# Kernel optimization log

Measured on AMD Instinct MI355X. Metric: run time of the kernel, lower is better.

Reference implementation:

```python
import jax, jax.numpy as jnp
import numpy as np
from jax import lax

BZ = 1024; ROI = 116; DIM = 116; FLAT = ROI * DIM
TOPK = 8; TEMP = 0.07; ALPHA = 0.1; A_COEF = 0.9; BETA = 2; EPS = 1e-5


def _leaky(v):
    return jnp.where(v >= 0, v, 0.2 * v)


def _bn2d(h, g, b):
    # training-mode BatchNorm1d on [N, C] (biased variance)
    m = h.mean(0)
    v = h.var(0)
    return (h - m) * lax.rsqrt(v + EPS) * g + b


def setup_inputs():
    key = jax.random.key(0)
    ks = jax.random.split(key, 16)
    def w(k, shape, s=0.05):
        return jax.random.normal(k, shape, jnp.float32) * s
    return {
        "x": jax.random.normal(ks[0], (BZ, ROI, DIM), jnp.float32),
        "pseudo": jax.random.normal(ks[1], (BZ, ROI, DIM), jnp.float32),
        "ages": jax.random.randint(ks[2], (BZ,), 0, 80, jnp.int32),
        "genders": jax.random.randint(ks[3], (BZ,), 0, 2, jnp.int32),
        "site": jax.random.randint(ks[4], (BZ, 4), 0, 10, jnp.int32),
        "fc_p_w": w(ks[5], (ROI, ROI)), "fc_p_b": jnp.zeros((ROI,), jnp.float32),
        "proj_w1": w(ks[6], (FLAT, ROI), 0.01), "proj_b1": jnp.zeros((ROI,), jnp.float32),
        "proj_w2": w(ks[7], (ROI, ROI)), "proj_b2": jnp.zeros((ROI,), jnp.float32),
        "gcn_w1": w(ks[8], (DIM, ROI)), "gcn_b1": jnp.zeros((ROI,), jnp.float32),
        "gcn_w2": w(ks[9], (ROI, ROI)), "gcn_b2": jnp.zeros((ROI,), jnp.float32),
        "gcn1_w": w(ks[10], (ROI, ROI)), "gcn1_b": jnp.zeros((ROI,), jnp.float32),
        "gcn2_w1": w(ks[11], (ROI, 64)), "gcn2_b1": jnp.zeros((64,), jnp.float32),
        "gcn2_w2": w(ks[12], (64, 8)), "gcn2_b2": jnp.zeros((8,), jnp.float32),
        "bn1_g": jnp.ones((ROI,), jnp.float32), "bn1_b": jnp.zeros((ROI,), jnp.float32),
        "bn2_g": jnp.ones((ROI,), jnp.float32), "bn2_b": jnp.zeros((ROI,), jnp.float32),
        "bn3_g": jnp.ones((ROI,), jnp.float32), "bn3_b": jnp.zeros((ROI,), jnp.float32),
    }


def _forward(x, pseudo, fc_p_w, fc_p_b, proj_w1, proj_b1, proj_w2, proj_b2,
             gcn_w1, gcn_b1, gcn_w2, gcn_b2, gcn1_w, gcn1_b,
             gcn2_w1, gcn2_b1, gcn2_w2, gcn2_b2,
             bn1_g, bn1_b, bn2_g, bn2_b, bn3_g, bn3_b,
             pos_idx, neg_idx, cond):
    bz = x.shape[0]
    pseudo = _leaky(pseudo @ fc_p_w + fc_p_b)
    x = x + pseudo                               # [bz, roi, dim]
    xf = x.reshape(bz, -1)                       # [bz, roi*dim]
    # contrastive head: Linear-ReLU-Linear, L2-normalize, cosine sim / temp
    p = jnp.maximum(xf @ proj_w1 + proj_b1, 0.0) @ proj_w2 + proj_b2
    pn = p / jnp.linalg.norm(p, axis=1, keepdims=True)
    sim = (pn @ pn.T) / TEMP                     # [bz, bz]
    sflat = sim.ravel()
    # -log(exp(pos)/(exp(pos)+exp(neg))) == softplus(neg - pos), truncated pairing
    loss = jnp.mean(jax.nn.softplus(sflat[neg_idx] - sflat[pos_idx]))
    sim_n = (sim - sim.min()) / (sim.max() - sim.min())
    # adjacency build: original does it in detached numpy -> stop_gradient
    xd = lax.stop_gradient(xf)
    sd = lax.stop_gradient(sim_n)
    sq = jnp.sum(xd * xd, axis=1)
    d2 = jnp.maximum(sq[:, None] + sq[None, :] - 2.0 * (xd @ xd.T), 0.0)
    fsim = jnp.exp(-ALPHA * jnp.sqrt(d2))
    total = fsim * (1.0 - sd) + sd
    dist = total * jnp.where(cond, A_COEF, 1.0 - A_COEF)
    vals, idxs = lax.top_k(dist, TOPK)           # row-wise top-8
    adj = jnp.zeros((bz, bz), jnp.float32).at[jnp.arange(bz)[:, None], idxs].set(vals)
    # GCN stack with flattened-feature message passing
    h = (adj @ xf).reshape(bz, ROI, DIM)
    h = _leaky(h @ gcn_w1 + gcn_b1) @ gcn_w2 + gcn_b2
    h = _bn2d(h.reshape(bz * ROI, -1), bn1_g, bn1_b).reshape(bz, ROI, -1)
    h = (adj @ h.reshape(bz, -1)).reshape(bz, ROI, -1)
    h = _leaky(h @ gcn1_w + gcn1_b)
    h = _bn2d(h.reshape(bz * ROI, -1), bn2_g, bn2_b).reshape(bz, ROI, -1)
    h = (adj @ h.reshape(bz, -1)).reshape(bz, ROI, -1)
    h = _leaky(_leaky(h @ gcn2_w1 + gcn2_b1) @ gcn2_w2 + gcn2_b2)  # [bz, roi, 8]
    # bn3: BatchNorm1d on [N, C=roi, L=8] -> per-channel over (N, L)
    m = h.mean((0, 2), keepdims=True)
    v = h.var((0, 2), keepdims=True)
    h = (h - m) * lax.rsqrt(v + EPS) * bn3_g[None, :, None] + bn3_b[None, :, None]
    return h, loss


def _masks(ages, genders, site):
    labels = np.asarray(site).argmax(1)
    eq = (labels[:, None] == labels[None, :]).ravel()
    pos_idx = np.nonzero(eq)[0]
    neg_idx = np.nonzero(~eq)[0]
    m = min(pos_idx.size, neg_idx.size)
    ag = np.asarray(ages); gd = np.asarray(genders)
    cond = (np.abs(ag[:, None] - ag[None, :]) <= BETA) & (gd[:, None] == gd[None, :])
    return jnp.asarray(pos_idx[:m]), jnp.asarray(neg_idx[:m]), jnp.asarray(cond)


def reference(x, pseudo, ages, genders, site, fc_p_w, fc_p_b, proj_w1, proj_b1,
              proj_w2, proj_b2, gcn_w1, gcn_b1, gcn_w2, gcn_b2, gcn1_w, gcn1_b,
              gcn2_w1, gcn2_b1, gcn2_w2, gcn2_b2, bn1_g, bn1_b, bn2_g, bn2_b,
              bn3_g, bn3_b):
    pos_idx, neg_idx, cond = _masks(ages, genders, site)
    return _forward(x, pseudo, fc_p_w, fc_p_b, proj_w1, proj_b1, proj_w2, proj_b2,
                    gcn_w1, gcn_b1, gcn_w2, gcn_b2, gcn1_w, gcn1_b,
                    gcn2_w1, gcn2_b1, gcn2_w2, gcn2_b2,
                    bn1_g, bn1_b, bn2_g, bn2_b, bn3_g, bn3_b,
                    pos_idx, neg_idx, cond)
```

## Files before the change

kernel.cpp:

```cpp
#include <hip/hip_runtime.h>
#include <math.h>

#define ROIN 116
#define NBZ 1024
#define LDF 128
#define SROW (ROIN*LDF)
#define NROWS (NBZ*ROIN)
#define ALPHA 0.1f
#define ACOEF 0.9f
#define BETAC 2
#define EPSBN 1e-5f
#define PZ 29
#define PCH 512
#define W1LD SROW
#define GX2 928
#define GX45 1856
#define GRAMZ 16
#define GRAMKS 928
#define NTRI 36

typedef __attribute__((ext_vector_type(8))) short bf16x8;
typedef __attribute__((ext_vector_type(4))) float f32x4;

__device__ __forceinline__ float leakyf(float v){ return v >= 0.f ? v : 0.2f*v; }

__device__ __forceinline__ short f2bf(float f){
    unsigned u = __builtin_bit_cast(unsigned, f);
    unsigned r = u + 0x7fffu + ((u >> 16) & 1u);
    return (short)(r >> 16);
}
__device__ __forceinline__ float bf2f(short h){
    unsigned u = ((unsigned)(unsigned short)h) << 16;
    return __builtin_bit_cast(float, u);
}


template<bool PERM>
__global__ void wt_conv(const float* __restrict__ W, short* __restrict__ hi,
                        short* __restrict__ lo, int K, int N)
{
    int idx = blockIdx.x * 256 + threadIdx.x;
    int n = idx >> 7, kp = idx & 127;
    int k = PERM ? ((kp & 7) * 16 + (kp >> 3)) : kp;
    float v = (n < N && k < K) ? W[(size_t)k * N + n] : 0.f;
    short h = f2bf(v);
    hi[idx] = h;
    lo[idx] = f2bf(v - bf2f(h));
}

__global__ void wt1_conv(const float* __restrict__ W, short* __restrict__ hi,
                         short* __restrict__ lo)
{
    int idx = blockIdx.x * 256 + threadIdx.x;
    int n = idx / W1LD, k = idx - n * W1LD;
    int r = k >> 7, d = k & 127;
    float v = (n < ROIN && d < ROIN) ? W[(size_t)(r * ROIN + d) * ROIN + n] : 0.f;
    short h = f2bf(v);
    hi[idx] = h;
    lo[idx] = f2bf(v - bf2f(h));
}

template<int EPI, int XTRA, bool PADK>
__global__ __launch_bounds__(512) void mfma_gemm_w(
    const float* __restrict__ A, const short* __restrict__ wt_hi,
    const short* __restrict__ wt_lo, const float* __restrict__ bias,
    const float* __restrict__ X, float* __restrict__ C,
    short* __restrict__ bfout, float* __restrict__ rsq,
    int LDA, int LDC)
{
    __shared__ short whi[128][136];
    __shared__ short wlo[128][136];
    const int tid = threadIdx.x;
    {
        int r = tid >> 2, q = tid & 3;
        const short* sh = wt_hi + r * 128 + q * 32;
        const short* sl = wt_lo + r * 128 + q * 32;
        #pragma unroll
        for (int i = 0; i < 4; ++i) {
            *(bf16x8*)(&whi[r][q * 32 + i * 8]) = *(const bf16x8*)(sh + i * 8);
            *(bf16x8*)(&wlo[r][q * 32 + i * 8]) = *(const bf16x8*)(sl + i * 8);
        }
    }
    __syncthreads();
    const int wave = tid >> 6, lane = tid & 63;
    const int m0 = blockIdx.x * 128 + wave * 16;
    const int rl = lane & 15, g = lane >> 4;
    const float* Arow = A + (size_t)(m0 + rl) * LDA;
    float av[4][8];
    #pragma unroll
    for (int s = 0; s < 4; ++s) {
        const int kk = s * 32 + g * 8;
        if (PADK || kk + 8 <= ROIN) {
            float4 p = *(const float4*)(Arow + kk);
            float4 q = *(const float4*)(Arow + kk + 4);
            av[s][0]=p.x; av[s][1]=p.y; av[s][2]=p.z; av[s][3]=p.w;
            av[s][4]=q.x; av[s][5]=q.y; av[s][6]=q.z; av[s][7]=q.w;
        } else if (kk + 4 <= ROIN) {
            float4 p = *(const float4*)(Arow + kk);
            av[s][0]=p.x; av[s][1]=p.y; av[s][2]=p.z; av[s][3]=p.w;
            av[s][4]=0.f; av[s][5]=0.f; av[s][6]=0.f; av[s][7]=0.f;
        } else {
            #pragma unroll
            for (int j = 0; j < 8; ++j) av[s][j] = 0.f;
        }
    }
    f32x4 acc[8];
    #pragma unroll
    for (int nf = 0; nf < 8; ++nf) acc[nf] = (f32x4){0.f,0.f,0.f,0.f};
    #pragma unroll
    for (int s = 0; s < 4; ++s) {
        const int kk = s * 32 + g * 8;
        bf16x8 ah, al;
        #pragma unroll
        for (int j = 0; j < 8; ++j) {
            short h = f2bf(av[s][j]); ah[j] = h;
            al[j] = f2bf(av[s][j] - bf2f(h));
        }
        #pragma unroll
        for (int nf = 0; nf < 8; ++nf) {
            const bf16x8 bh = *(const bf16x8*)(&whi[nf * 16 + rl][kk]);
            const bf16x8 bl = *(const bf16x8*)(&wlo[nf * 16 + rl][kk]);
            acc[nf] = __builtin_amdgcn_mfma_f32_16x16x32_bf16(ah, bh, acc[nf], 0, 0, 0);
            acc[nf] = __builtin_amdgcn_mfma_f32_16x16x32_bf16(al, bh, acc[nf], 0, 0, 0);
            acc[nf] = __builtin_amdgcn_mfma_f32_16x16x32_bf16(ah, bl, acc[nf], 0, 0, 0);
        }
    }
    const int cm = g * 4;
    float rq[4] = {0.f, 0.f, 0.f, 0.f};
    bf16x8 bfv[4];
    #pragma unroll
    for (int nf = 0; nf < 8; ++nf) {
        int n = nf * 16 + rl;
        float bb = (n < ROIN) ? bias[n] : 0.f;
        #pragma unroll
        for (int j = 0; j < 4; ++j) {
            int m = m0 + cm + j;
            size_t idx = (size_t)m * LDC + n;
            float v = 0.f;
            if (n < ROIN) {
                v = acc[nf][j] + bb;
                if (EPI == 3) v = leakyf(v);
                else if (EPI == 4) v = X[(size_t)m * LDA + n] + leakyf(v);
            }
            if (n < LDC) C[idx] = v;
            if (XTRA == 1) { bfv[j][nf] = f2bf(v); rq[j] += v * v; }
        }
    }
    if (XTRA == 1) {
        #pragma unroll
        for (int j = 0; j < 4; ++j)
            *(bf16x8*)(&bfout[(size_t)(m0 + cm + j) * LDF + rl * 8]) = bfv[j];
        #pragma unroll
        for (int j = 0; j < 4; ++j) {
            rq[j] += __shfl_xor(rq[j], 1);
            rq[j] += __shfl_xor(rq[j], 2);
            rq[j] += __shfl_xor(rq[j], 4);
            rq[j] += __shfl_xor(rq[j], 8);
        }
        if (rl == 0) {
            #pragma unroll
            for (int j = 0; j < 4; ++j) rsq[m0 + cm + j] = rq[j];
        }
    }
}

template<int XTRA, bool FOLD>
__global__ __launch_bounds__(512, 4) void mfma_gemm_wg_h(
    const float* __restrict__ vals, const int* __restrict__ idxs,
    const short* __restrict__ feat, const float* __restrict__ sbP,
    const float* __restrict__ tbP,
    const short* __restrict__ wt_hi, const short* __restrict__ wt_lo,
    const float* __restrict__ bias, short* __restrict__ outH,
    float* __restrict__ statp)
{
    __shared__ short whi[128][136];
    __shared__ short wlo[128][136];
    __shared__ float st[(XTRA == 2) ? 8 : 1][2][128];
    const int tid = threadIdx.x;
    {
        int r = tid >> 2, q = tid & 3;
        const short* sh = wt_hi + r * 128 + q * 32;
        const short* sl = wt_lo + r * 128 + q * 32;
        #pragma unroll
        for (int i = 0; i < 4; ++i) {
            *(bf16x8*)(&whi[r][q * 32 + i * 8]) = *(const bf16x8*)(sh + i * 8);
            *(bf16x8*)(&wlo[r][q * 32 + i * 8]) = *(const bf16x8*)(sl + i * 8);
        }
    }
    __syncthreads();
    const int wave = tid >> 6, lane = tid & 63;
    const int m0 = blockIdx.x * 128 + wave * 16;
    const int rl = lane & 15, g = lane >> 4;
    const int m = m0 + rl;
    const unsigned bz = (unsigned)m / 116u;
    const int r = m - (int)bz * 116;
    float vv[8]; const short* fp[8];
    #pragma unroll
    for (int k = 0; k < 8; ++k) {
        vv[k] = vals[bz * 8 + k];
        int ixk = idxs[bz * 8 + k];
        fp[k] = feat + ((size_t)ixk * 116 + r) * 128;
    }
    float wsum = 0.f;
    if (FOLD) {
        #pragma unroll
        for (int k = 0; k < 8; ++k) wsum += vv[k];
    }
    f32x4 acc[8];
    #pragma unroll
    for (int nf = 0; nf < 8; ++nf) acc[nf] = (f32x4){0.f,0.f,0.f,0.f};
    bf16x8 xb[8], xn[8];
    #pragma unroll
    for (int k = 0; k < 8; ++k) xb[k] = *(const bf16x8*)(fp[k] + g * 8);
    #pragma unroll
    for (int s = 0; s < 4; ++s) {
        const int kk = s * 32 + g * 8;
        if (s < 3) {
            #pragma unroll
            for (int k = 0; k < 8; ++k) xn[k] = *(const bf16x8*)(fp[k] + kk + 32);
        }
        float av[8] = {0.f,0.f,0.f,0.f,0.f,0.f,0.f,0.f};
        #pragma unroll
        for (int k = 0; k < 8; ++k) {
            const float vk = vv[k];
            #pragma unroll
            for (int j = 0; j < 8; ++j) av[j] = fmaf(vk, bf2f(xb[k][j]), av[j]);
        }
        if (FOLD) {
            #pragma unroll
            for (int j = 0; j < 8; ++j)
                av[j] = sbP[kk + j] * av[j] + wsum * tbP[kk + j];
        }
        bf16x8 ah, al;
        #pragma unroll
        for (int j = 0; j < 8; ++j) {
            short h = f2bf(av[j]); ah[j] = h;
            al[j] = f2bf(av[j] - bf2f(h));
        }
        __builtin_amdgcn_s_setprio(1);
        #pragma unroll
        for (int nf = 0; nf < 8; ++nf) {
            const bf16x8 bh = *(const bf16x8*)(&whi[nf * 16 + rl][kk]);
            const bf16x8 bl = *(const bf16x8*)(&wlo[nf * 16 + rl][kk]);
            acc[nf] = __builtin_amdgcn_mfma_f32_16x16x32_bf16(ah, bh, acc[nf], 0, 0, 0);
            acc[nf] = __builtin_amdgcn_mfma_f32_16x16x32_bf16(al, bh, acc[nf], 0, 0, 0);
            acc[nf] = __builtin_amdgcn_mfma_f32_16x16x32_bf16(ah, bl, acc[nf], 0, 0, 0);
        }
        __builtin_amdgcn_s_setprio(0);
        #pragma unroll
        for (int k = 0; k < 8; ++k) xb[k] = xn[k];
    }
    const int cm = g * 4;
    bf16x8 bfv[4];
    #pragma unroll
    for (int nf = 0; nf < 8; ++nf) {
        int n = nf * 16 + rl;
        float c1 = 0.f, c2 = 0.f;
        float bb = (n < ROIN) ? bias[n] : 0.f;
        #pragma unroll
        for (int j = 0; j < 4; ++j) {
            float v = 0.f;
            if (n < ROIN) v = leakyf(acc[nf][j] + bb);
            bfv[j][nf] = f2bf(v);
            if (XTRA == 2) { c1 += v; c2 += v * v; }
        }
        if (XTRA == 2) {
            c1 += __shfl_xor(c1, 16); c1 += __shfl_xor(c1, 32);
            c2 += __shfl_xor(c2, 16); c2 += __shfl_xor(c2, 32);
            if (lane < 16) { st[wave][0][n & 127] = c1; st[wave][1][n & 127] = c2; }
        }
    }
    #pragma unroll
    for (int j = 0; j < 4; ++j)
        *(bf16x8*)(&outH[(size_t)(m0 + cm + j) * LDF + rl * 8]) = bfv[j];
    if (XTRA == 2) {
        __syncthreads();
        if (tid < 232) {
            int sel = tid < 116 ? 0 : 1;
            int c = sel ? tid - 116 : tid;
            float s = 0.f;
            #pragma unroll
            for (int wv = 0; wv < 8; ++wv) s += st[wv][sel][c];
            statp[(size_t)(sel * 116 + c) * GX2 + blockIdx.x] = s;
        }
    }
}

__global__ __launch_bounds__(512) void mfma_gemm_bA(
    const short* __restrict__ A,
    const short* __restrict__ wt_hi, const short* __restrict__ wt_lo,
    const float* __restrict__ bias, short* __restrict__ outH,
    float* __restrict__ statp)
{
    __shared__ short whi[128][136];
    __shared__ short wlo[128][136];
    __shared__ float st[8][2][128];
    const int tid = threadIdx.x;
    {
        int r = tid >> 2, q = tid & 3;
        const short* sh = wt_hi + r * 128 + q * 32;
        const short* sl = wt_lo + r * 128 + q * 32;
        #pragma unroll
        for (int i = 0; i < 4; ++i) {
            *(bf16x8*)(&whi[r][q * 32 + i * 8]) = *(const bf16x8*)(sh + i * 8);
            *(bf16x8*)(&wlo[r][q * 32 + i * 8]) = *(const bf16x8*)(sl + i * 8);
        }
    }
    __syncthreads();
    const int wave = tid >> 6, lane = tid & 63;
    const int m0 = blockIdx.x * 128 + wave * 16;
    const int rl = lane & 15, g = lane >> 4;
    const short* Arow = A + (size_t)(m0 + rl) * LDF;
    bf16x8 av[4];
    #pragma unroll
    for (int s = 0; s < 4; ++s) av[s] = *(const bf16x8*)(Arow + s * 32 + g * 8);
    f32x4 acc[8];
    #pragma unroll
    for (int nf = 0; nf < 8; ++nf) acc[nf] = (f32x4){0.f,0.f,0.f,0.f};
    #pragma unroll
    for (int s = 0; s < 4; ++s) {
        const int kk = s * 32 + g * 8;
        const bf16x8 ah = av[s];
        #pragma unroll
        for (int nf = 0; nf < 8; ++nf) {
            const bf16x8 bh = *(const bf16x8*)(&whi[nf * 16 + rl][kk]);
            const bf16x8 bl = *(const bf16x8*)(&wlo[nf * 16 + rl][kk]);
            acc[nf] = __builtin_amdgcn_mfma_f32_16x16x32_bf16(ah, bh, acc[nf], 0, 0, 0);
            acc[nf] = __builtin_amdgcn_mfma_f32_16x16x32_bf16(ah, bl, acc[nf], 0, 0, 0);
        }
    }
    const int cm = g * 4;
    bf16x8 bfv[4];
    #pragma unroll
    for (int nf = 0; nf < 8; ++nf) {
        int n = nf * 16 + rl;
        float c1 = 0.f, c2 = 0.f;
        float bb = (n < ROIN) ? bias[n] : 0.f;
        #pragma unroll
        for (int j = 0; j < 4; ++j) {
            float v = 0.f;
            if (n < ROIN) v = acc[nf][j] + bb;
            bfv[j][nf] = f2bf(v);
            c1 += v; c2 += v * v;
        }
        c1 += __shfl_xor(c1, 16); c1 += __shfl_xor(c1, 32);
        c2 += __shfl_xor(c2, 16); c2 += __shfl_xor(c2, 32);
        if (lane < 16) { st[wave][0][n & 127] = c1; st[wave][1][n & 127] = c2; }
    }
    #pragma unroll
    for (int j = 0; j < 4; ++j)
        *(bf16x8*)(&outH[(size_t)(m0 + cm + j) * LDF + rl * 8]) = bfv[j];
    __syncthreads();
    if (tid < 232) {
        int sel = tid < 116 ? 0 : 1;
        int c = sel ? tid - 116 : tid;
        float s = 0.f;
        #pragma unroll
        for (int wv = 0; wv < 8; ++wv) s += st[wv][sel][c];
        statp[(size_t)(sel * 116 + c) * GX2 + blockIdx.x] = s;
    }
}

__global__ __launch_bounds__(256) void mfma_gemm45_wg_h(
    const float* __restrict__ vals, const int* __restrict__ idxs,
    const short* __restrict__ feat, const float* __restrict__ sbP,
    const float* __restrict__ tbP,
    const short* __restrict__ w5h, const short* __restrict__ w5l,
    const float* __restrict__ b5,
    const short* __restrict__ w6h, const short* __restrict__ w6l,
    const float* __restrict__ b6,
    float* __restrict__ C)
{
    __shared__ short s5h[64][136], s5l[64][136];
    __shared__ short s6h[16][136], s6l[16][136];
    __shared__ float c1s[4][16][76];
    const int tid = threadIdx.x;
    {
        int r = tid >> 2, q = tid & 3;
        const short* sh = w5h + r * 128 + q * 32;
        const short* sl = w5l + r * 128 + q * 32;
        #pragma unroll
        for (int i = 0; i < 4; ++i) {
            *(bf16x8*)(&s5h[r][q * 32 + i * 8]) = *(const bf16x8*)(sh + i * 8);
            *(bf16x8*)(&s5l[r][q * 32 + i * 8]) = *(const bf16x8*)(sl + i * 8);
        }
        if (tid < 64) {
            int r6 = tid >> 2, q6 = tid & 3;
            const short* sh6 = w6h + r6 * 128 + q6 * 32;
            const short* sl6 = w6l + r6 * 128 + q6 * 32;
            #pragma unroll
            for (int i = 0; i < 4; ++i) {
                *(bf16x8*)(&s6h[r6][q6 * 32 + i * 8]) = *(const bf16x8*)(sh6 + i * 8);
                *(bf16x8*)(&s6l[r6][q6 * 32 + i * 8]) = *(const bf16x8*)(sl6 + i * 8);
            }
        }
    }
    __syncthreads();
    const int wave = tid >> 6, lane = tid & 63;
    const int m0 = blockIdx.x * 64 + wave * 16;
    const int rl = lane & 15, g = lane >> 4;
    const int m = m0 + rl;
    const unsigned bz = (unsigned)m / 116u;
    const int r = m - (int)bz * 116;
    float vv[8]; const short* fp[8];
    #pragma unroll
    for (int k = 0; k < 8; ++k) {
        vv[k] = vals[bz * 8 + k];
        int ixk = idxs[bz * 8 + k];
        fp[k] = feat + ((size_t)ixk * 116 + r) * 128;
    }
    float wsum = 0.f;
    #pragma unroll
    for (int k = 0; k < 8; ++k) wsum += vv[k];
    f32x4 acc[4];
    #pragma unroll
    for (int nf = 0; nf < 4; ++nf) acc[nf] = (f32x4){0.f,0.f,0.f,0.f};
    bf16x8 xb[8], xn[8];
    #pragma unroll
    for (int k = 0; k < 8; ++k) xb[k] = *(const bf16x8*)(fp[k] + g * 8);
    #pragma unroll
    for (int s = 0; s < 4; ++s) {
        const int kk = s * 32 + g * 8;
        if (s < 3) {
            #pragma unroll
            for (int k = 0; k < 8; ++k) xn[k] = *(const bf16x8*)(fp[k] + kk + 32);
        }
        float av[8] = {0.f,0.f,0.f,0.f,0.f,0.f,0.f,0.f};
        #pragma unroll
        for (int k = 0; k < 8; ++k) {
            const float vk = vv[k];
            #pragma unroll
            for (int j = 0; j < 8; ++j) av[j] = fmaf(vk, bf2f(xb[k][j]), av[j]);
        }
        #pragma unroll
        for (int j = 0; j < 8; ++j)
            av[j] = sbP[kk + j] * av[j] + wsum * tbP[kk + j];
        bf16x8 ah, al;
        #pragma unroll
        for (int j = 0; j < 8; ++j) {
            short h = f2bf(av[j]); ah[j] = h;
            al[j] = f2bf(av[j] - bf2f(h));
        }
        __builtin_amdgcn_s_setprio(1);
        #pragma unroll
        for (int nf = 0; nf < 4; ++nf) {
            const bf16x8 bh = *(const bf16x8*)(&s5h[nf * 16 + rl][kk]);
            const bf16x8 bl = *(const bf16x8*)(&s5l[nf * 16 + rl][kk]);
            acc[nf] = __builtin_amdgcn_mfma_f32_16x16x32_bf16(ah, bh, acc[nf], 0, 0, 0);
            acc[nf] = __builtin_amdgcn_mfma_f32_16x16x32_bf16(al, bh, acc[nf], 0, 0, 0);
            acc[nf] = __builtin_amdgcn_mfma_f32_16x16x32_bf16(ah, bl, acc[nf], 0, 0, 0);
        }
        __builtin_amdgcn_s_setprio(0);
        #pragma unroll
        for (int k = 0; k < 8; ++k) xb[k] = xn[k];
    }
    const int cm = g * 4;
    #pragma unroll
    for (int nf = 0; nf < 4; ++nf) {
        int n = nf * 16 + rl;
        float bb = b5[n];
        #pragma unroll
        for (int j = 0; j < 4; ++j)
            c1s[wave][cm + j][n] = leakyf(acc[nf][j] + bb);
    }
    f32x4 acc2 = {0.f,0.f,0.f,0.f};
    #pragma unroll
    for (int s = 0; s < 2; ++s) {
        const int kk = s * 32 + g * 8;
        float4 p = *(const float4*)(&c1s[wave][rl][kk]);
        float4 q = *(const float4*)(&c1s[wave][rl][kk + 4]);
        float a2[8] = {p.x, p.y, p.z, p.w, q.x, q.y, q.z, q.w};
        bf16x8 ah, al;
        #pragma unroll
        for (int j = 0; j < 8; ++j) {
            short h = f2bf(a2[j]); ah[j] = h;
            al[j] = f2bf(a2[j] - bf2f(h));
        }
        const bf16x8 bh = *(const bf16x8*)(&s6h[rl][kk]);
        const bf16x8 bl = *(const bf16x8*)(&s6l[rl][kk]);
        acc2 = __builtin_amdgcn_mfma_f32_16x16x32_bf16(ah, bh, acc2, 0, 0, 0);
        acc2 = __builtin_amdgcn_mfma_f32_16x16x32_bf16(al, bh, acc2, 0, 0, 0);
        acc2 = __builtin_amdgcn_mfma_f32_16x16x32_bf16(ah, bl, acc2, 0, 0, 0);
    }
    if (rl < 8) {
        float bb = b6[rl];
        #pragma unroll
        for (int j = 0; j < 4; ++j) {
            float v = leakyf(acc2[j] + bb);
            C[(size_t)(m0 + cm + j) * 8 + rl] = v;
        }
    }
}

__global__ void bn_final_st_p(const float* __restrict__ statp, const float* __restrict__ g,
                              const float* __restrict__ bta, float* __restrict__ sbP,
                              float* __restrict__ tbP, int cnt)
{
    int c = blockIdx.x, tid = threadIdx.x;
    int pc = (c & 15) * 8 + (c >> 4);
    if (c >= ROIN) { if (tid == 0) { sbP[pc] = 0.f; tbP[pc] = 0.f; } return; }
    float a1 = 0.f, a2 = 0.f;
    for (int i = tid; i < cnt; i += 256) {
        a1 += statp[(size_t)c * cnt + i];
        a2 += statp[(size_t)(116 + c) * cnt + i];
    }
    __shared__ float r1[256], r2[256];
    r1[tid] = a1; r2[tid] = a2; __syncthreads();
    for (int off = 128; off > 0; off >>= 1) {
        if (tid < off) { r1[tid] += r1[tid + off]; r2[tid] += r2[tid + off]; }
        __syncthreads();
    }
    if (tid == 0) {
        float mean = r1[0] / (float)NROWS;
        float var = r2[0] / (float)NROWS - mean * mean;
        float rstd = 1.f / sqrtf(var + EPSBN);
        float s = rstd * g[c];
        sbP[pc] = s;
        tbP[pc] = bta[c] - mean * s;
    }
}

__global__ void sq_reduce(const float* __restrict__ rsq, float* __restrict__ sq)
{
    int i = blockIdx.x * 256 + threadIdx.x;
    if (i >= NBZ) return;
    const float* p = rsq + (size_t)i * ROIN;
    float s = 0.f;
    #pragma unroll 4
    for (int r = 0; r < ROIN; ++r) s += p[r];
    sq[i] = s;
}

__global__ __launch_bounds__(256) void mfma_proj1(
    const float* __restrict__ A, const short* __restrict__ wt_hi,
    const short* __restrict__ wt_lo, float* __restrict__ part)
{
    const int wave = threadIdx.x >> 6, lane = threadIdx.x & 63;
    const int m0 = blockIdx.x * 64 + wave * 16;
    const int rl = lane & 15, g = lane >> 4;
    const int kbase = blockIdx.z * PCH;
    const float* Arow = A + (size_t)(m0 + rl) * SROW;
    f32x4 acc[8];
    #pragma unroll
    for (int nf = 0; nf < 8; ++nf) acc[nf] = (f32x4){0.f,0.f,0.f,0.f};
    for (int s = 0; s < 16; ++s) {
        const int kk = kbase + s * 32 + g * 8;
        float4 p = *(const float4*)(Arow + kk);
        float4 q = *(const float4*)(Arow + kk + 4);
        float av[8] = {p.x, p.y, p.z, p.w, q.x, q.y, q.z, q.w};
        bf16x8 ah, al;
        #pragma unroll
        for (int j = 0; j < 8; ++j) {
            short h = f2bf(av[j]); ah[j] = h;
            al[j] = f2bf(av[j] - bf2f(h));
        }
        #pragma unroll
        for (int nf = 0; nf < 8; ++nf) {
            size_t boff = (size_t)(nf * 16 + rl) * W1LD + kk;
            bf16x8 bh = *(const bf16x8*)(wt_hi + boff);
            bf16x8 bl = *(const bf16x8*)(wt_lo + boff);
            acc[nf] = __builtin_amdgcn_mfma_f32_16x16x32_bf16(ah, bh, acc[nf], 0, 0, 0);
            acc[nf] = __builtin_amdgcn_mfma_f32_16x16x32_bf16(al, bh, acc[nf], 0, 0, 0);
            acc[nf] = __builtin_amdgcn_mfma_f32_16x16x32_bf16(ah, bl, acc[nf], 0, 0, 0);
        }
    }
    float* Cb = part + (size_t)blockIdx.z * NBZ * ROIN;
    const int cm = g * 4;
    #pragma unroll
    for (int nf = 0; nf < 8; ++nf) {
        int n = nf * 16 + rl;
        if (n < ROIN) {
            #pragma unroll
            for (int j = 0; j < 4; ++j)
                Cb[(size_t)(m0 + cm + j) * ROIN + n] = acc[nf][j];
        }
    }
}

__global__ void proj_reduce(const float* __restrict__ ppart,
                            const float* __restrict__ bias, float* __restrict__ t1)
{
    int e = blockIdx.x * 256 + threadIdx.x;
    if (e >= NBZ * ROIN) return;
    int n = e % ROIN;
    float s = 0.f;
    for (int z = 0; z < PZ; ++z) s += ppart[(size_t)z * NBZ * ROIN + e];
    t1[e] = fmaxf(s + bias[n], 0.f);
}

__global__ __launch_bounds__(256) void gemm_nt_sym(
    const float* __restrict__ A, float* __restrict__ C, int M, int K, float scale)
{
    if ((int)blockIdx.y < (int)blockIdx.x) return;
    __shared__ float As[16][65];
    __shared__ float Bs[16][65];
    const int tid = threadIdx.x;
    const int m0 = blockIdx.x * 64;
    const int n0 = blockIdx.y * 64;
    const int tm4 = (tid >> 4) * 4;
    const int tn4 = (tid & 15) * 4;
    const int rA  = tid >> 2;
    const int kbA = (tid & 3) * 4;
    float acc[4][4] = {};
    for (int kt = 0; kt < K; kt += 16) {
        int kg = kt + kbA;
        if (kg + 4 <= K) {
            float4 va = *(const float4*)(A + (size_t)(m0 + rA) * K + kg);
            As[kbA + 0][rA] = va.x; As[kbA + 1][rA] = va.y;
            As[kbA + 2][rA] = va.z; As[kbA + 3][rA] = va.w;
            float4 vb = *(const float4*)(A + (size_t)(n0 + rA) * K + kg);
            Bs[kbA + 0][rA] = vb.x; Bs[kbA + 1][rA] = vb.y;
            Bs[kbA + 2][rA] = vb.z; Bs[kbA + 3][rA] = vb.w;
        } else {
            #pragma unroll
            for (int kk = 0; kk < 4; ++kk) {
                int kgg = kg + kk;
                As[kbA + kk][rA] = (kgg < K) ? A[(size_t)(m0 + rA) * K + kgg] : 0.f;
                Bs[kbA + kk][rA] = (kgg < K) ? A[(size_t)(n0 + rA) * K + kgg] : 0.f;
            }
        }
        __syncthreads();
        #pragma unroll
        for (int k = 0; k < 16; ++k) {
            float a[4], b[4];
            #pragma unroll
            for (int i = 0; i < 4; ++i) a[i] = As[k][tm4 + i];
            #pragma unroll
            for (int j = 0; j < 4; ++j) b[j] = Bs[k][tn4 + j];
            #pragma unroll
            for (int i = 0; i < 4; ++i)
                #pragma unroll
                for (int j = 0; j < 4; ++j)
                    acc[i][j] = fmaf(a[i], b[j], acc[i][j]);
        }
        __syncthreads();
    }
    #pragma unroll
    for (int i = 0; i < 4; ++i) {
        int m = m0 + tm4 + i;
        #pragma unroll
        for (int j = 0; j < 4; ++j) {
            int n = n0 + tn4 + j;
            float v = acc[i][j] * scale;
            C[(size_t)m * M + n] = v;
            C[(size_t)n * M + m] = v;
        }
    }
}

__global__ __launch_bounds__(256) void gram_mfma(
    const short* __restrict__ Xh, float* __restrict__ gpart)
{
    const int id = blockIdx.x;
    const int wg = (id & 7) * 72 + (id >> 3);
    const int z = wg / 36;
    const int tri = wg - z * 36;
    int bx = 0;
    #pragma unroll
    for (int b = 1; b < 8; ++b) {
        int base = b * 8 - (b * (b - 1)) / 2;
        if (base <= tri) bx = b;
    }
    const int by = tri - (bx * 8 - (bx * (bx - 1)) / 2) + bx;
    const int k0 = z * GRAMKS;
    const int wave = threadIdx.x >> 6, lane = threadIdx.x & 63;
    const int wr = wave >> 1, wc = wave & 1;
    const int row = lane & 15, koff = (lane >> 4) * 8;
    const short* Ap[4]; const short* Bp[4];
    #pragma unroll
    for (int i = 0; i < 4; ++i) {
        Ap[i] = Xh + (size_t)(bx * 128 + wr * 64 + i * 16 + row) * SROW;
        Bp[i] = Xh + (size_t)(by * 128 + wc * 64 + i * 16 + row) * SROW;
    }
    f32x4 acc[4][4];
    #pragma unroll
    for (int i = 0; i < 4; ++i)
        #pragma unroll
        for (int j = 0; j < 4; ++j) acc[i][j] = (f32x4){0.f,0.f,0.f,0.f};
    bf16x8 a[4], b[4];
    {
        int kk = k0 + koff;
        #pragma unroll
        for (int i = 0; i < 4; ++i) {
            a[i] = *(const bf16x8*)(Ap[i] + kk);
            b[i] = *(const bf16x8*)(Bp[i] + kk);
        }
    }
    for (int k = k0 + 32; k < k0 + GRAMKS; k += 32) {
        bf16x8 an[4], bn[4];
        int kk = k + koff;
        #pragma unroll
        for (int i = 0; i < 4; ++i) {
            an[i] = *(const bf16x8*)(Ap[i] + kk);
            bn[i] = *(const bf16x8*)(Bp[i] + kk);
        }
        #pragma unroll
        for (int i = 0; i < 4; ++i)
            #pragma unroll
            for (int j = 0; j < 4; ++j)
                acc[i][j] = __builtin_amdgcn_mfma_f32_16x16x32_bf16(a[i], b[j], acc[i][j], 0, 0, 0);
        #pragma unroll
        for (int i = 0; i < 4; ++i) { a[i] = an[i]; b[i] = bn[i]; }
    }
    #pragma unroll
    for (int i = 0; i < 4; ++i)
        #pragma unroll
        for (int j = 0; j < 4; ++j)
            acc[i][j] = __builtin_amdgcn_mfma_f32_16x16x32_bf16(a[i], b[j], acc[i][j], 0, 0, 0);
    float* Cb = gpart + ((size_t)z * NTRI + tri) * 16384;
    const int crow = (lane >> 4) * 4;
    const int ccol = lane & 15;
    #pragma unroll
    for (int i = 0; i < 4; ++i) {
        #pragma unroll
        for (int j = 0; j < 4; ++j) {
            int cl = wc * 64 + j * 16 + ccol;
            #pragma unroll
            for (int jj = 0; jj < 4; ++jj) {
                int rl2 = wr * 64 + i * 16 + crow + jj;
                Cb[(size_t)rl2 * 128 + cl] = acc[i][j][jj];
            }
        }
    }
}

__global__ void gram_reduce_dist(const float* __restrict__ gpart,
                                 const float* __restrict__ sim, const float* __restrict__ sq,
                                 const int* __restrict__ ages, const int* __restrict__ genders,
                                 const float* __restrict__ fscal, float* __restrict__ G)
{
    const int t = blockIdx.x;
    int bx = 0;
    #pragma unroll
    for (int b = 1; b < 8; ++b) {
        int base = b * 8 - (b * (b - 1)) / 2;
        if (base <= t) bx = b;
    }
    const int by = t - (bx * 8 - (bx * (bx - 1)) / 2) + bx;
    int e = blockIdx.y * 1024 + threadIdx.x * 4;
    float sx = 0.f, sy = 0.f, sz = 0.f, sw = 0.f;
    for (int z = 0; z < GRAMZ; ++z) {
        float4 v = *(const float4*)(gpart + ((size_t)z * NTRI + t) * 16384 + e);
        sx += v.x; sy += v.y; sz += v.z; sw += v.w;
    }
    const int i = bx * 128 + (e >> 7), j0 = by * 128 + (e & 127);
    const float smin = fscal[0], smax = fscal[1];
    const float inv = 1.f / (smax - smin);
    const float sqi = sq[i];
    const int agei = ages[i], geni = genders[i];
    float4 simv = *(const float4*)(sim + ((size_t)i << 10) + j0);
    float gs[4] = {sx, sy, sz, sw};
    float sms[4] = {simv.x, simv.y, simv.z, simv.w};
    float out[4];
    #pragma unroll
    for (int c = 0; c < 4; ++c) {
        int j = j0 + c;
        float sn = (sms[c] - smin) * inv;
        float d2 = fmaxf(sqi + sq[j] - 2.f * gs[c], 0.f);
        float fs = expf(-ALPHA * sqrtf(d2));
        float total = fs * (1.f - sn) + sn;
        int da = agei - ages[j]; if (da < 0) da = -da;
        bool cond = (da <= BETAC) && (geni == genders[j]);
        out[c] = total * (cond ? ACOEF : 1.f - ACOEF);
    }
    float4 o = {out[0], out[1], out[2], out[3]};
    *(float4*)(G + ((size_t)i << 10) + j0) = o;
    #pragma unroll
    for (int c = 0; c < 4; ++c)
        G[((size_t)(j0 + c) << 10) + i] = out[c];
}

__global__ void rownorm(float* __restrict__ p)
{
    int row = blockIdx.x, t = threadIdx.x;
    __shared__ float red[128];
    float x = 0.f, v = 0.f;
    if (t < ROIN) { x = p[row * ROIN + t]; v = x * x; }
    red[t] = v; __syncthreads();
    for (int off = 64; off > 0; off >>= 1) { if (t < off) red[t] += red[t + off]; __syncthreads(); }
    float inv = 1.f / sqrtf(red[0]);
    if (t < ROIN) p[row * ROIN + t] = x * inv;
}

__global__ void minmax_part(const float* __restrict__ sim, float* __restrict__ mm)
{
    int t = threadIdx.x, b = blockIdx.x;
    float mn = 1e30f, mx = -1e30f;
    for (size_t i = (size_t)b * 256 + t; i < 1048576u; i += 512u * 256u) {
        float v = sim[i]; mn = fminf(mn, v); mx = fmaxf(mx, v);
    }
    __shared__ float smn[256], smx[256];
    smn[t] = mn; smx[t] = mx; __syncthreads();
    for (int off = 128; off > 0; off >>= 1) {
        if (t < off) { smn[t] = fminf(smn[t], smn[t + off]); smx[t] = fmaxf(smx[t], smx[t + off]); }
        __syncthreads();
    }
    if (t == 0) { mm[b] = smn[0]; mm[512 + b] = smx[0]; }
}
__global__ void minmax_final(const float* __restrict__ mm, float* __restrict__ fscal)
{
    int t = threadIdx.x;
    __shared__ float smn[512], smx[512];
    smn[t] = mm[t]; smx[t] = mm[512 + t]; __syncthreads();
    for (int off = 256; off > 0; off >>= 1) {
        if (t < off) { smn[t] = fminf(smn[t], smn[t + off]); smx[t] = fmaxf(smx[t], smx[t + off]); }
        __syncthreads();
    }
    if (t == 0) { fscal[0] = smn[0]; fscal[1] = smx[0]; }
}

__global__ void labels_k(const int* __restrict__ site, int* __restrict__ labels)
{
    int i = blockIdx.x * 256 + threadIdx.x;
    if (i >= NBZ) return;
    int best = site[4 * i], bi = 0;
    #pragma unroll
    for (int k = 1; k < 4; ++k) { int v = site[4 * i + k]; if (v > best) { best = v; bi = k; } }
    labels[i] = bi;
}

__global__ void rowcnt_k(const int* __restrict__ labels, int* __restrict__ rowcnt)
{
    int i = blockIdx.x * 256 + threadIdx.x;
    if (i >= NBZ) return;
    int li = labels[i], c = 0;
    for (int j = 0; j < NBZ; ++j) c += (labels[j] == li);
    rowcnt[i] = c;
}

__global__ __launch_bounds__(1024) void scan_k(const int* __restrict__ rowcnt,
                                               int* __restrict__ rowoff, int* __restrict__ iscal)
{
    __shared__ int s[1024];
    int t = threadIdx.x;
    int c = rowcnt[t];
    s[t] = c; __syncthreads();
    for (int off = 1; off < 1024; off <<= 1) {
        int v = (t >= off) ? s[t - off] : 0;
        __syncthreads();
        s[t] += v;
        __syncthreads();
    }
    rowoff[t] = s[t] - c;
    if (t == 1023) {
        int npos = s[1023];
        int nneg = 1024 * 1024 - npos;
        iscal[0] = npos;
        iscal[1] = (npos < nneg) ? npos : nneg;
    }
}

__global__ void pair_scatter(const int* __restrict__ labels, const int* __restrict__ rowoff,
                             const int* __restrict__ iscal, const float* __restrict__ sim,
                             float* __restrict__ posval, float* __restrict__ negval)
{
    int row = blockIdx.x, t = threadIdx.x;
    int m = iscal[1];
    int li = labels[row];
    int j0 = t * 4;
    int eq[4]; int c = 0;
    #pragma unroll
    for (int kk = 0; kk < 4; ++kk) { eq[kk] = (labels[j0 + kk] == li); c += eq[kk]; }
    __shared__ int s[256];
    s[t] = c; __syncthreads();
    for (int off = 1; off < 256; off <<= 1) {
        int v = (t >= off) ? s[t - off] : 0;
        __syncthreads();
        s[t] += v;
        __syncthreads();
    }
    int r = rowoff[row] + s[t] - c;
    size_t base = (size_t)row * 1024;
    #pragma unroll
    for (int kk = 0; kk < 4; ++kk) {
        size_t f = base + j0 + kk;
        float v = sim[f];
        if (eq[kk]) { if (r < m) posval[r] = v; r++; }
        else { long nr = (long)f - r; if (nr < m) negval[nr] = v; }
    }
}

__global__ void loss_part(const float* __restrict__ posval, const float* __restrict__ negval,
                          const int* __restrict__ iscal, float* __restrict__ lp)
{
    int m = iscal[1];
    int t = threadIdx.x, b = blockIdx.x;
    float s = 0.f;
    for (int k = b * 256 + t; k < m; k += 1024 * 256) {
        float d = negval[k] - posval[k];
        s += fmaxf(d, 0.f) + log1pf(expf(-fabsf(d)));
    }
    __shared__ float red[256];
    red[t] = s; __syncthreads();
    for (int off = 128; off > 0; off >>= 1) { if (t < off) red[t] += red[t + off]; __syncthreads(); }
    if (t == 0) lp[b] = red[0];
}

__global__ void loss_final(const float* __restrict__ lp, const int* __restrict__ iscal,
                           float* __restrict__ outp)
{
    int t = threadIdx.x;
    double s = 0.0;
    for (int k = t; k < 1024; k += 256) s += (double)lp[k];
    __shared__ double red[256];
    red[t] = s; __syncthreads();
    for (int off = 128; off > 0; off >>= 1) { if (t < off) red[t] += red[t + off]; __syncthreads(); }
    if (t == 0) {
        int m = iscal[1]; if (m < 1) m = 1;
        outp[0] = (float)(red[0] / (double)m);
    }
}

__global__ void topk8(const float* __restrict__ dist, float* __restrict__ topv, int* __restrict__ topi)
{
    int row = blockIdx.x, t = threadIdx.x;
    __shared__ float sv[1024];
    __shared__ float rv[256];
    __shared__ int   ri[256];
    for (int j = t; j < 1024; j += 256) sv[j] = dist[(size_t)row * 1024 + j];
    __syncthreads();
    for (int k = 0; k < 8; ++k) {
        float bv = -1e30f; int bi = 1 << 20;
        for (int j = t; j < 1024; j += 256) {
            float x = sv[j];
            if (x > bv || (x == bv && j < bi)) { bv = x; bi = j; }
        }
        rv[t] = bv; ri[t] = bi;
        __syncthreads();
        for (int s = 128; s > 0; s >>= 1) {
            if (t < s) {
                float ov = rv[t + s]; int oi = ri[t + s];
                if (ov > rv[t] || (ov == rv[t] && oi < ri[t])) { rv[t] = ov; ri[t] = oi; }
            }
            __syncthreads();
        }
        if (t == 0) { topv[row * 8 + k] = rv[0]; topi[row * 8 + k] = ri[0]; sv[ri[0]] = -1e30f; }
        __syncthreads();
    }
}

__global__ void bn3_k(const float* __restrict__ X, const float* __restrict__ g,
                      const float* __restrict__ bta, float* __restrict__ out)
{
    int c = blockIdx.x, t = threadIdx.x;
    float s = 0.f, s2 = 0.f;
    for (int k = t; k < 8192; k += 256) {
        int n = k >> 3, l = k & 7;
        float v = X[(size_t)n * 928 + c * 8 + l];
        s += v; s2 += v * v;
    }
    __shared__ float rs[256], rs2[256];
    rs[t] = s; rs2[t] = s2; __syncthreads();
    for (int off = 128; off > 0; off >>= 1) {
        if (t < off) { rs[t] += rs[t + off]; rs2[t] += rs2[t + off]; }
        __syncthreads();
    }
    __shared__ float sm, sr;
    if (t == 0) {
        float mean = rs[0] / 8192.f;
        float var = rs2[0] / 8192.f - mean * mean;
        sm = mean; sr = 1.f / sqrtf(var + EPSBN);
    }
    __syncthreads();
    float mean = sm, rstd = sr, gg = g[c], bb = bta[c];
    for (int k = t; k < 8192; k += 256) {
        int n = k >> 3, l = k & 7;
        size_t idx = (size_t)n * 928 + c * 8 + l;
        out[idx] = (X[idx] - mean) * rstd * gg + bb;
    }
}

extern "C" void kernel_launch(void* const* d_in, const int* in_sizes, int n_in,
                              void* d_out, int out_size, void* d_ws, size_t ws_size,
                              hipStream_t stream)
{
    const float* x        = (const float*)d_in[0];
    const float* pseudo   = (const float*)d_in[1];
    const int*   ages     = (const int*)d_in[2];
    const int*   genders  = (const int*)d_in[3];
    const int*   site     = (const int*)d_in[4];
    const float* fc_p_w   = (const float*)d_in[5];
    const float* fc_p_b   = (const float*)d_in[6];
    const float* proj_w1  = (const float*)d_in[7];
    const float* proj_b1  = (const float*)d_in[8];
    const float* proj_w2  = (const float*)d_in[9];
    const float* proj_b2  = (const float*)d_in[10];
    const float* gcn_w1   = (const float*)d_in[11];
    const float* gcn_b1   = (const float*)d_in[12];
    const float* gcn_w2   = (const float*)d_in[13];
    const float* gcn_b2   = (const float*)d_in[14];
    const float* gcn1_w   = (const float*)d_in[15];
    const float* gcn1_b   = (const float*)d_in[16];
    const float* gcn2_w1  = (const float*)d_in[17];
    const float* gcn2_b1  = (const float*)d_in[18];
    const float* gcn2_w2  = (const float*)d_in[19];
    const float* gcn2_b2  = (const float*)d_in[20];
    const float* bn1_g    = (const float*)d_in[21];
    const float* bn1_b    = (const float*)d_in[22];
    const float* bn2_g    = (const float*)d_in[23];
    const float* bn2_b    = (const float*)d_in[24];
    const float* bn3_g    = (const float*)d_in[25];
    const float* bn3_b    = (const float*)d_in[26];
    float* dout = (float*)d_out;

    char* w = (char*)d_ws;
    size_t off = 0;
    auto carve = [&](size_t bytes) { char* p = w + off; off = (off + bytes + 255) & ~(size_t)255; return p; };
    float* xf     = (float*)carve((size_t)NROWS * LDF * 4);
    float* hA     = (float*)carve((size_t)NROWS * LDF * 4);
    float* hB     = (float*)carve((size_t)NROWS * LDF * 4);
    float* G      = (float*)carve(1048576u * 4);
    float* simb   = (float*)carve(1048576u * 4);
    float* t1     = (float*)carve((size_t)NBZ * ROIN * 4);
    float* pbuf   = (float*)carve((size_t)NBZ * ROIN * 4);
    float* sq     = (float*)carve(4096);
    float* rsq    = (float*)carve((size_t)NROWS * 4);
    int*   labels = (int*)carve(4096);
    int*   rowcnt = (int*)carve(4096);
    int*   rowoff = (int*)carve(4096);
    int*   iscal  = (int*)carve(256);
    float* fscal  = (float*)carve(256);
    float* posval = (float*)carve(524288u * 4);
    float* negval = (float*)carve(524288u * 4);
    float* lpart  = (float*)carve(4096);
    float* mmpart = (float*)carve(4096);
    float* topv   = (float*)carve(32768);
    int*   topi   = (int*)carve(32768);
    float* statp  = (float*)carve((size_t)232 * GX2 * 4);
    float* sbAp   = (float*)carve(512);
    float* tbAp   = (float*)carve(512);
    float* sbBp   = (float*)carve(512);
    float* tbBp   = (float*)carve(512);
    short* wt1_hi = (short*)carve((size_t)128 * W1LD * 2);
    short* wt1_lo = (short*)carve((size_t)128 * W1LD * 2);
    short* wts    = (short*)carve((size_t)7 * 2 * 16384 * 2);
    float* ppart  = hA;
    float* gpart  = hA;
    short* xfh    = (short*)((char*)hB + (16u << 20));
    short* actH1  = (short*)hA;
    short* actH2  = (short*)hB;
    short* actH3  = (short*)hA;
    float* h45    = hB;

    auto wt_hi = [&](int i) { return wts + (size_t)i * 2 * 16384; };
    auto wt_lo = [&](int i) { return wts + (size_t)i * 2 * 16384 + 16384; };

    wt1_conv<<<(128 * W1LD) / 256, 256, 0, stream>>>(proj_w1, wt1_hi, wt1_lo);
    wt_conv<false><<<64, 256, 0, stream>>>(fc_p_w,  wt_hi(0), wt_lo(0), 116, 116);
    wt_conv<false><<<64, 256, 0, stream>>>(proj_w2, wt_hi(1), wt_lo(1), 116, 116);
    wt_conv<true ><<<64, 256, 0, stream>>>(gcn_w1,  wt_hi(2), wt_lo(2), 116, 116);
    wt_conv<true ><<<64, 256, 0, stream>>>(gcn_w2,  wt_hi(3), wt_lo(3), 116, 116);
    wt_conv<true ><<<64, 256, 0, stream>>>(gcn1_w,  wt_hi(4), wt_lo(4), 116, 116);
    wt_conv<true ><<<64, 256, 0, stream>>>(gcn2_w1, wt_hi(5), wt_lo(5), 116, 64);
    wt_conv<false><<<64, 256, 0, stream>>>(gcn2_w2, wt_hi(6), wt_lo(6), 64, 8);

    mfma_gemm_w<4, 1, false><<<GX2, 512, 0, stream>>>(pseudo, wt_hi(0), wt_lo(0), fc_p_b, x, xf,
                                                      xfh, rsq, ROIN, LDF);
    sq_reduce<<<4, 256, 0, stream>>>(rsq, sq);

    mfma_proj1<<<dim3(16, 1, PZ), 256, 0, stream>>>(xf, wt1_hi, wt1_lo, ppart);
    proj_reduce<<<(NBZ * ROIN + 255) / 256, 256, 0, stream>>>(ppart, proj_b1, t1);
    mfma_gemm_w<1, 0, false><<<8, 512, 0, stream>>>(t1, wt_hi(1), wt_lo(1), proj_b2, nullptr, pbuf,
                                                    nullptr, nullptr, ROIN, ROIN);
    rownorm<<<NBZ, 128, 0, stream>>>(pbuf);

    gemm_nt_sym<<<dim3(16, 16, 1), 256, 0, stream>>>(pbuf, simb, NBZ, ROIN, 1.f / 0.07f);

    labels_k<<<4, 256, 0, stream>>>(site, labels);
    rowcnt_k<<<4, 256, 0, stream>>>(labels, rowcnt);
    scan_k<<<1, 1024, 0, stream>>>(rowcnt, rowoff, iscal);
    pair_scatter<<<NBZ, 256, 0, stream>>>(labels, rowoff, iscal, simb, posval, negval);
    loss_part<<<1024, 256, 0, stream>>>(posval, negval, iscal, lpart);
    loss_final<<<1, 256, 0, stream>>>(lpart, iscal, dout + (size_t)NBZ * ROIN * 8);

    minmax_part<<<512, 256, 0, stream>>>(simb, mmpart);
    minmax_final<<<1, 512, 0, stream>>>(mmpart, fscal);
    gram_mfma<<<NTRI * GRAMZ, 256, 0, stream>>>(xfh, gpart);
    gram_reduce_dist<<<dim3(NTRI, 16), 256, 0, stream>>>(gpart, simb, sq, ages, genders, fscal, G);
    topk8<<<NBZ, 256, 0, stream>>>(G, topv, topi);

    mfma_gemm_wg_h<0, false><<<GX2, 512, 0, stream>>>(topv, topi, xfh, nullptr, nullptr,
                                                      wt_hi(2), wt_lo(2), gcn_b1, actH1, nullptr);
    mfma_gemm_bA<<<GX2, 512, 0, stream>>>(actH1, wt_hi(3), wt_lo(3), gcn_b2, actH2, statp);
    bn_final_st_p<<<128, 256, 0, stream>>>(statp, bn1_g, bn1_b, sbAp, tbAp, GX2);

    mfma_gemm_wg_h<2, true><<<GX2, 512, 0, stream>>>(topv, topi, actH2, sbAp, tbAp,
                                                     wt_hi(4), wt_lo(4), gcn1_b, actH3, statp);
    bn_final_st_p<<<128, 256, 0, stream>>>(statp, bn2_g, bn2_b, sbBp, tbBp, GX2);

    mfma_gemm45_wg_h<<<GX45, 256, 0, stream>>>(topv, topi, actH3, sbBp, tbBp,
                                               wt_hi(5), wt_lo(5), gcn2_b1,
                                               wt_hi(6), wt_lo(6), gcn2_b2, h45);

    bn3_k<<<116, 256, 0, stream>>>(h45, bn3_g, bn3_b, dout);
}
```

Before: 588.4 us.

## Store fused x as bf16 hi/lo split and feed proj1 directly

After: 553.3 us. 6.0% less time.

```diff
diff --git a/kernel.cpp b/kernel.cpp
--- a/kernel.cpp
+++ b/kernel.cpp
@@ -53,7 +53,8 @@
 {
     int idx = blockIdx.x * 256 + threadIdx.x;
     int n = idx / W1LD, k = idx - n * W1LD;
-    int r = k >> 7, d = k & 127;
+    int r = k >> 7, dp = k & 127;
+    int d = (dp & 7) * 16 + (dp >> 3);
     float v = (n < ROIN && d < ROIN) ? W[(size_t)(r * ROIN + d) * ROIN + n] : 0.f;
     short h = f2bf(v);
     hi[idx] = h;
@@ -65,7 +66,7 @@
     const float* __restrict__ A, const short* __restrict__ wt_hi,
     const short* __restrict__ wt_lo, const float* __restrict__ bias,
     const float* __restrict__ X, float* __restrict__ C,
-    short* __restrict__ bfout, float* __restrict__ rsq,
+    short* __restrict__ bfout, short* __restrict__ bflo, float* __restrict__ rsq,
     int LDA, int LDC)
 {
     __shared__ short whi[128][136];
@@ -126,30 +127,33 @@
         }
     }
     const int cm = g * 4;
-    float rq[4] = {0.f, 0.f, 0.f, 0.f};
-    bf16x8 bfv[4];
-    #pragma unroll
-    for (int nf = 0; nf < 8; ++nf) {
-        int n = nf * 16 + rl;
-        float bb = (n < ROIN) ? bias[n] : 0.f;
+    if (XTRA == 1) {
+        bf16x8 bfh[4], bfl[4];
+        float rq[4] = {0.f, 0.f, 0.f, 0.f};
+        #pragma unroll
+        for (int nf = 0; nf < 8; ++nf) {
+            int n = nf * 16 + rl;
+            float bb = (n < ROIN) ? bias[n] : 0.f;
+            #pragma unroll
+            for (int j = 0; j < 4; ++j) {
+                int m = m0 + cm + j;
+                float v = 0.f;
+                if (n < ROIN) {
+                    v = acc[nf][j] + bb;
+                    if (EPI == 3) v = leakyf(v);
+                    else if (EPI == 4) v = X[(size_t)m * LDA + n] + leakyf(v);
+                }
+                short h = f2bf(v);
+                bfh[j][nf] = h;
+                bfl[j][nf] = f2bf(v - bf2f(h));
+                rq[j] += v * v;
+            }
+        }
         #pragma unroll
         for (int j = 0; j < 4; ++j) {
-            int m = m0 + cm + j;
-            size_t idx = (size_t)m * LDC + n;
-            float v = 0.f;
-            if (n < ROIN) {
-                v = acc[nf][j] + bb;
-                if (EPI == 3) v = leakyf(v);
-                else if (EPI == 4) v = X[(size_t)m * LDA + n] + leakyf(v);
-            }
-            if (n < LDC) C[idx] = v;
-            if (XTRA == 1) { bfv[j][nf] = f2bf(v); rq[j] += v * v; }
-        }
-    }
-    if (XTRA == 1) {
-        #pragma unroll
-        for (int j = 0; j < 4; ++j)
-            *(bf16x8*)(&bfout[(size_t)(m0 + cm + j) * LDF + rl * 8]) = bfv[j];
+            *(bf16x8*)(&bfout[(size_t)(m0 + cm + j) * LDF + rl * 8]) = bfh[j];
+            *(bf16x8*)(&bflo[(size_t)(m0 + cm + j) * LDF + rl * 8]) = bfl[j];
+        }
         #pragma unroll
         for (int j = 0; j < 4; ++j) {
             rq[j] += __shfl_xor(rq[j], 1);
@@ -160,6 +164,23 @@
         if (rl == 0) {
             #pragma unroll
             for (int j = 0; j < 4; ++j) rsq[m0 + cm + j] = rq[j];
+        }
+    } else {
+        #pragma unroll
+        for (int nf = 0; nf < 8; ++nf) {
+            int n = nf * 16 + rl;
+            float bb = (n < ROIN) ? bias[n] : 0.f;
+            #pragma unroll
+            for (int j = 0; j < 4; ++j) {
+                int m = m0 + cm + j;
+                float v = 0.f;
+                if (n < ROIN) {
+                    v = acc[nf][j] + bb;
+                    if (EPI == 3) v = leakyf(v);
+                    else if (EPI == 4) v = X[(size_t)m * LDA + n] + leakyf(v);
+                }
+                if (n < LDC) C[(size_t)m * LDC + n] = v;
+            }
         }
     }
 }
@@ -532,28 +553,23 @@
 }
 
 __global__ __launch_bounds__(256) void mfma_proj1(
-    const float* __restrict__ A, const short* __restrict__ wt_hi,
-    const short* __restrict__ wt_lo, float* __restrict__ part)
+    const short* __restrict__ XH, const short* __restrict__ XL,
+    const short* __restrict__ wt_hi, const short* __restrict__ wt_lo,
+    float* __restrict__ part)
 {
     const int wave = threadIdx.x >> 6, lane = threadIdx.x & 63;
     const int m0 = blockIdx.x * 64 + wave * 16;
     const int rl = lane & 15, g = lane >> 4;
     const int kbase = blockIdx.z * PCH;
-    const float* Arow = A + (size_t)(m0 + rl) * SROW;
+    const short* Ah = XH + (size_t)(m0 + rl) * SROW;
+    const short* Al = XL + (size_t)(m0 + rl) * SROW;
     f32x4 acc[8];
     #pragma unroll
     for (int nf = 0; nf < 8; ++nf) acc[nf] = (f32x4){0.f,0.f,0.f,0.f};
     for (int s = 0; s < 16; ++s) {
         const int kk = kbase + s * 32 + g * 8;
-        float4 p = *(const float4*)(Arow + kk);
-        float4 q = *(const float4*)(Arow + kk + 4);
-        float av[8] = {p.x, p.y, p.z, p.w, q.x, q.y, q.z, q.w};
-        bf16x8 ah, al;
-        #pragma unroll
-        for (int j = 0; j < 8; ++j) {
-            short h = f2bf(av[j]); ah[j] = h;
-            al[j] = f2bf(av[j] - bf2f(h));
-        }
+        const bf16x8 ah = *(const bf16x8*)(Ah + kk);
+        const bf16x8 al = *(const bf16x8*)(Al + kk);
         #pragma unroll
         for (int nf = 0; nf < 8; ++nf) {
             size_t boff = (size_t)(nf * 16 + rl) * W1LD + kk;
@@ -1006,7 +1022,7 @@
     char* w = (char*)d_ws;
     size_t off = 0;
     auto carve = [&](size_t bytes) { char* p = w + off; off = (off + bytes + 255) & ~(size_t)255; return p; };
-    float* xf     = (float*)carve((size_t)NROWS * LDF * 4);
+    float* xfb    = (float*)carve((size_t)NROWS * LDF * 4);
     float* hA     = (float*)carve((size_t)NROWS * LDF * 4);
     float* hB     = (float*)carve((size_t)NROWS * LDF * 4);
     float* G      = (float*)carve(1048576u * 4);
@@ -1034,9 +1050,10 @@
     short* wt1_hi = (short*)carve((size_t)128 * W1LD * 2);
     short* wt1_lo = (short*)carve((size_t)128 * W1LD * 2);
     short* wts    = (short*)carve((size_t)7 * 2 * 16384 * 2);
+    short* xfh    = (short*)xfb;
+    short* xfl    = (short*)xfb + (size_t)NROWS * LDF;
     float* ppart  = hA;
     float* gpart  = hA;
-    short* xfh    = (short*)((char*)hB + (16u << 20));
     short* actH1  = (short*)hA;
     short* actH2  = (short*)hB;
     short* actH3  = (short*)hA;
@@ -1054,14 +1071,14 @@
     wt_conv<true ><<<64, 256, 0, stream>>>(gcn2_w1, wt_hi(5), wt_lo(5), 116, 64);
     wt_conv<false><<<64, 256, 0, stream>>>(gcn2_w2, wt_hi(6), wt_lo(6), 64, 8);
 
-    mfma_gemm_w<4, 1, false><<<GX2, 512, 0, stream>>>(pseudo, wt_hi(0), wt_lo(0), fc_p_b, x, xf,
-                                                      xfh, rsq, ROIN, LDF);
+    mfma_gemm_w<4, 1, false><<<GX2, 512, 0, stream>>>(pseudo, wt_hi(0), wt_lo(0), fc_p_b, x,
+                                                      nullptr, xfh, xfl, rsq, ROIN, LDF);
     sq_reduce<<<4, 256, 0, stream>>>(rsq, sq);
 
-    mfma_proj1<<<dim3(16, 1, PZ), 256, 0, stream>>>(xf, wt1_hi, wt1_lo, ppart);
+    mfma_proj1<<<dim3(16, 1, PZ), 256, 0, stream>>>(xfh, xfl, wt1_hi, wt1_lo, ppart);
     proj_reduce<<<(NBZ * ROIN + 255) / 256, 256, 0, stream>>>(ppart, proj_b1, t1);
     mfma_gemm_w<1, 0, false><<<8, 512, 0, stream>>>(t1, wt_hi(1), wt_lo(1), proj_b2, nullptr, pbuf,
-                                                    nullptr, nullptr, ROIN, ROIN);
+                                                    nullptr, nullptr, nullptr, ROIN, ROIN);
     rownorm<<<NBZ, 128, 0, stream>>>(pbuf);
 
     gemm_nt_sym<<<dim3(16, 16, 1), 256, 0, stream>>>(pbuf, simb, NBZ, ROIN, 1.f / 0.07f);
```
